# Performance work log

Hardware: AMD Instinct MI355X
Metric: run time of the kernel (lower is better)

The kernel has to match this reference:

```python
import jax, jax.numpy as jnp
import numpy as np

N = 4096
FEAT = 64


def _pairwise_dist(x):
    # x: [N, F] -> symmetric [N, N] Euclidean distance matrix, zero diagonal
    sq = jnp.sum(x * x, axis=-1)
    d2 = sq[:, None] + sq[None, :] - 2.0 * (x @ x.T)
    d = jnp.sqrt(jnp.maximum(d2, 0.0))
    return d * (1.0 - jnp.eye(x.shape[0], dtype=x.dtype))


def setup_inputs() -> dict:
    key = jax.random.key(0)
    k1, k2 = jax.random.split(key)
    x1 = jax.random.normal(k1, (N, FEAT), dtype=jnp.float32)
    x2 = jax.random.normal(k2, (N, FEAT), dtype=jnp.float32)
    return {"d1": _pairwise_dist(x1), "d2": _pairwise_dist(x2)}


def _mst_edges(d):
    # Prim's algorithm, O(N^2). For a distance matrix with generic (distinct)
    # entries the MST is unique and its N-1 edges are exactly the 0-dim
    # persistence pairs returned by the union-find PersistentHomologyCalculation.
    n = d.shape[0]
    INF = jnp.asarray(jnp.finfo(d.dtype).max, d.dtype)
    in_tree = jnp.zeros((n,), dtype=bool).at[0].set(True)
    min_dist = d[0]                       # best edge weight into the tree per node
    parent = jnp.zeros((n,), dtype=jnp.int32)  # tree endpoint of that best edge

    def step(carry, _):
        in_tree, min_dist, parent = carry
        masked = jnp.where(in_tree, INF, min_dist)
        j = jnp.argmin(masked).astype(jnp.int32)
        edge = jnp.stack([parent[j], j])  # (tree node, new node)
        in_tree = in_tree.at[j].set(True)
        dj = d[j]
        upd = (dj < min_dist) & (~in_tree)
        min_dist = jnp.where(upd, dj, min_dist)
        parent = jnp.where(upd, j, parent)
        return (in_tree, min_dist, parent), edge

    _, edges = jax.lax.scan(step, (in_tree, min_dist, parent), None, length=n - 1)
    return edges  # [N-1, 2] int32; d is symmetric so pair order is irrelevant


def reference(d1, d2):
    # Pairings are computed on detached CPU copies in the original -> no grad
    p1 = _mst_edges(jax.lax.stop_gradient(d1))
    p2 = jax.lax.stop_gradient(_mst_edges(jax.lax.stop_gradient(d2)))
    sig1 = d1[p1[:, 0], p1[:, 1]]
    sig2 = d2[p2[:, 0], p2[:, 1]]
    # match_edges == 'symmetric'
    sig1_2 = d2[p1[:, 0], p1[:, 1]]
    sig2_1 = d1[p2[:, 0], p2[:, 1]]
    return jnp.sum((sig1 - sig1_2) ** 2) + jnp.sum((sig2 - sig2_1) ** 2)
```

## Files before the change

kernel.cpp:

```cpp
#include <hip/hip_runtime.h>
#include <stdint.h>


#define N        4096
#define NROUNDS  12

typedef unsigned long long u64;
typedef uint32_t u32;

#define INFK (~0ull)

struct Ws {
    u64 best[2][N];
    u32 comp[2][N];
    u32 edges[2][N];
    u32 ncomp[2];
    u32 pad[14];
    u64 bm[2][N * 64];
};

__device__ __forceinline__ u64 umin64(u64 a, u64 b) { return a < b ? a : b; }

__device__ __forceinline__ u64 shfl_xor_u64(u64 x, int off) {
    u32 lo = (u32)x, hi = (u32)(x >> 32);
    lo = (u32)__shfl_xor((int)lo, off, 64);
    hi = (u32)__shfl_xor((int)hi, off, 64);
    return ((u64)hi << 32) | lo;
}

__launch_bounds__(256, 8)
__global__ void scanA_k(const float* __restrict__ d1, const float* __restrict__ d2,
                        Ws* __restrict__ ws) {
    const int m = blockIdx.x >> 10;
    const int wave = threadIdx.x >> 6, lane = threadIdx.x & 63;
    const int v = ((blockIdx.x & 1023) << 2) + wave;
    const float4* __restrict__ row4 = (const float4*)((m ? d2 : d1) + (size_t)v * N);

    const u32 uv = (u32)v;
    u64 bmin = INFK;
    #pragma unroll
    for (int j = 0; j < 16; ++j) {
        const int c = lane + 64 * j;
        float4 w = row4[c];
        const u32 c0 = (u32)(4 * c);
        if (c0 + 0 != uv) bmin = umin64(bmin, (((u64)__float_as_uint(w.x)) << 12) | (c0 + 0));
        if (c0 + 1 != uv) bmin = umin64(bmin, (((u64)__float_as_uint(w.y)) << 12) | (c0 + 1));
        if (c0 + 2 != uv) bmin = umin64(bmin, (((u64)__float_as_uint(w.z)) << 12) | (c0 + 2));
        if (c0 + 3 != uv) bmin = umin64(bmin, (((u64)__float_as_uint(w.w)) << 12) | (c0 + 3));
    }
    ws->bm[m][(size_t)v * 64 + lane] = bmin;

    u64 rowmin = bmin;
    #pragma unroll
    for (int off = 1; off <= 32; off <<= 1)
        rowmin = umin64(rowmin, shfl_xor_u64(rowmin, off));

    if (lane == 0) {
        u32 u  = (u32)rowmin & 0xFFFu;
        u64 wb = rowmin >> 12;
        u32 lo = min(uv, u), hi = max(uv, u);
        ws->best[m][v]  = (wb << 24) | ((u64)lo << 12) | (u64)hi;
        ws->comp[m][v]  = uv;
        ws->edges[m][v] = (uv << 12) | uv;
    }
    if (threadIdx.x == 0 && (blockIdx.x & 1023) == 0)
        ws->ncomp[m] = (u32)N;
}

__launch_bounds__(256, 8)
__global__ void scan2_k(const float* __restrict__ d1, const float* __restrict__ d2,
                        Ws* __restrict__ ws) {
    const int m = blockIdx.x >> 10;
    if (ws->ncomp[m] <= 1u) return;
    const int wave = threadIdx.x >> 6, lane = threadIdx.x & 63;
    const int v = ((blockIdx.x & 1023) << 2) + wave;

    const float* __restrict__ dm = m ? d2 : d1;
    const u32*   __restrict__ cm = ws->comp[m];
    u64* __restrict__ bmrow = ws->bm[m] + (size_t)v * 64;

    const u32 cv = cm[v];
    u64 key = bmrow[lane];
    bool cross = false;
    if (key != INFK) cross = (cm[(u32)key & 0xFFFu] != cv);

    u64 kb = cross ? key : INFK;
    #pragma unroll
    for (int off = 1; off <= 32; off <<= 1)
        kb = umin64(kb, shfl_xor_u64(kb, off));

    const bool need = (!cross) && (key < kb);
    u64 nm = INFK;
    if (need) {
        const float4* __restrict__ row4 = (const float4*)(dm + (size_t)v * N);
        const uint4*  __restrict__ c4   = (const uint4*)cm;
        #pragma unroll
        for (int j = 0; j < 16; ++j) {
            const int c = lane + 64 * j;
            float4 w = row4[c];
            uint4 cu = c4[c];
            u32 c0 = (u32)(4 * c);
            if (cu.x != cv) nm = umin64(nm, (((u64)__float_as_uint(w.x)) << 12) | (c0 + 0));
            if (cu.y != cv) nm = umin64(nm, (((u64)__float_as_uint(w.y)) << 12) | (c0 + 1));
            if (cu.z != cv) nm = umin64(nm, (((u64)__float_as_uint(w.z)) << 12) | (c0 + 2));
            if (cu.w != cv) nm = umin64(nm, (((u64)__float_as_uint(w.w)) << 12) | (c0 + 3));
        }
        bmrow[lane] = nm;
    }
    u64 kb2 = need ? nm : INFK;
    #pragma unroll
    for (int off = 1; off <= 32; off <<= 1)
        kb2 = umin64(kb2, shfl_xor_u64(kb2, off));

    u64 fin = umin64(kb, kb2);
    if (lane == 0 && fin != INFK) {
        u32 u  = (u32)fin & 0xFFFu;
        u64 wb = fin >> 12;
        u32 lo = min((u32)v, u), hi = max((u32)v, u);
        u64 g  = (wb << 24) | ((u64)lo << 12) | (u64)hi;
        if (g < ws->best[m][cv])
            atomicMin(&ws->best[m][cv], g);
    }
}

__launch_bounds__(256, 8)
__global__ void scanF_k(const float* __restrict__ d1, const float* __restrict__ d2,
                        Ws* __restrict__ ws, int first) {
    const int m = blockIdx.x >> 10;
    if (!first && ws->ncomp[m] <= 1u) return;
    const int wave = threadIdx.x >> 6, lane = threadIdx.x & 63;
    const int v = ((blockIdx.x & 1023) << 2) + wave;
    const float* __restrict__ dm = m ? d2 : d1;
    const u32*   __restrict__ cm = ws->comp[m];
    const float4* __restrict__ row4 = (const float4*)(dm + (size_t)v * N);
    const uint4*  __restrict__ c4   = (const uint4*)cm;
    const u32 cv = first ? (u32)v : cm[v];
    u64 kmin = INFK;
    #pragma unroll
    for (int j = 0; j < 16; ++j) {
        const int c = lane + 64 * j;
        float4 w = row4[c];
        uint4 cu;
        if (!first) cu = c4[c];
        const u32 c0 = (u32)(4 * c);
        bool x0, x1, x2, x3;
        if (first) {
            x0 = (c0+0 != cv); x1 = (c0+1 != cv); x2 = (c0+2 != cv); x3 = (c0+3 != cv);
        } else {
            x0 = (cu.x != cv); x1 = (cu.y != cv); x2 = (cu.z != cv); x3 = (cu.w != cv);
        }
        if (x0) kmin = umin64(kmin, (((u64)__float_as_uint(w.x)) << 12) | (c0 + 0));
        if (x1) kmin = umin64(kmin, (((u64)__float_as_uint(w.y)) << 12) | (c0 + 1));
        if (x2) kmin = umin64(kmin, (((u64)__float_as_uint(w.z)) << 12) | (c0 + 2));
        if (x3) kmin = umin64(kmin, (((u64)__float_as_uint(w.w)) << 12) | (c0 + 3));
    }
    #pragma unroll
    for (int off = 1; off <= 32; off <<= 1)
        kmin = umin64(kmin, shfl_xor_u64(kmin, off));
    if (lane == 0 && kmin != INFK) {
        u32 u  = (u32)kmin & 0xFFFu;
        u64 wb = kmin >> 12;
        u32 lo = min((u32)v, u), hi = max((u32)v, u);
        u64 g  = (wb << 24) | ((u64)lo << 12) | (u64)hi;
        if (first) {
            ws->best[m][v]  = g;
            ws->comp[m][v]  = (u32)v;
            ws->edges[m][v] = ((u32)v << 12) | (u32)v;
        } else if (g < ws->best[m][cv]) {
            atomicMin(&ws->best[m][cv], g);
        }
    }
    if (first && threadIdx.x == 0 && (blockIdx.x & 1023) == 0)
        ws->ncomp[m] = (u32)N;
}

__launch_bounds__(1024, 1)
__global__ void hook_k(const float* __restrict__ d1, const float* __restrict__ d2,
                       Ws* __restrict__ ws, float* __restrict__ out, int fin) {
    const int m = blockIdx.x;
    const int tid = threadIdx.x;
    const int lane = tid & 63, wave = tid >> 6;

    __shared__ u32 compL[N];
    __shared__ u32 nxtA[N];
    __shared__ u32 nxtB[N];
    __shared__ u32 red[16];
    __shared__ float fpart[16];

    if (ws->ncomp[m] > 1u) {
        u32* __restrict__ gcomp = ws->comp[m];
        u64* __restrict__ best  = ws->best[m];

        {
            uint4* dst = (uint4*)compL;
            const uint4* src = (const uint4*)gcomp;
            if (tid < N / 4) dst[tid] = src[tid];
        }
        __syncthreads();

        bool isroot[4];
        u64  bkey[4];

        #pragma unroll
        for (int k = 0; k < 4; ++k) {
            int i = tid + k * 1024;
            u32 x = (u32)i;
            bool r = (compL[i] == (u32)i);
            isroot[k] = r;
            u64 g = 0;
            if (r) {
                g = best[i];
                u32 lo = (u32)(g >> 12) & 0xFFFu;
                u32 hi = (u32)g & 0xFFFu;
                u32 cl = compL[lo], ch = compL[hi];
                x = (cl == (u32)i) ? ch : cl;
            }
            bkey[k] = g;
            nxtA[i] = x;
        }
        __syncthreads();

        #pragma unroll
        for (int k = 0; k < 4; ++k) {
            int i = tid + k * 1024;
            u32 nn = (u32)i;
            if (isroot[k]) {
                u32 o = nxtA[i];
                bool mutual = (nxtA[o] == (u32)i);
                nn = (mutual && ((u32)i < o)) ? (u32)i : o;
                if (nn != (u32)i)
                    ws->edges[m][i] = (u32)(bkey[k] & 0xFFFFFFu);
            }
            nxtB[i] = nn;
        }
        __syncthreads();

        for (int s = 0; s < 12; ++s) {
            u32 changed = 0;
            #pragma unroll
            for (int k = 0; k < 4; ++k) {
                int i = tid + k * 1024;
                u32 a = nxtB[i];
                u32 t = nxtB[a];
                if (t != a) changed = 1u;
                nxtB[i] = t;
            }
            if (!__syncthreads_or((int)changed)) break;
        }

        u32 cnt = 0;
        #pragma unroll
        for (int k = 0; k < 4; ++k) {
            int i = tid + k * 1024;
            if (isroot[k] && nxtB[i] == (u32)i) cnt++;
        }
        #pragma unroll
        for (int off = 32; off >= 1; off >>= 1) cnt += (u32)__shfl_down((int)cnt, off, 64);
        if (lane == 0) red[wave] = cnt;
        __syncthreads();

        #pragma unroll
        for (int k = 0; k < 4; ++k) {
            int i = tid + k * 1024;
            gcomp[i] = nxtB[compL[i]];
            if (isroot[k]) best[i] = INFK;
        }
        if (tid == 0) {
            u32 t = 0;
            #pragma unroll
            for (int w = 0; w < 16; ++w) t += red[w];
            ws->ncomp[m] = t;
        }
    }

    if (fin) {
        __syncthreads();
        float acc = 0.f;
        #pragma unroll
        for (int k = 0; k < 4; ++k) {
            int i = tid + k * 1024;
            u32 pk = ws->edges[m][i];
            u32 lo = (pk >> 12) & 0xFFFu, hi = pk & 0xFFFu;
            size_t off = (size_t)lo * N + hi;
            float df = d1[off] - d2[off];
            acc += df * df;
        }
        #pragma unroll
        for (int off = 32; off >= 1; off >>= 1) acc += __shfl_down(acc, off, 64);
        if (lane == 0) fpart[wave] = acc;
        __syncthreads();
        if (tid == 0) {
            float t = 0.f;
            #pragma unroll
            for (int w = 0; w < 16; ++w) t += fpart[w];
            atomicAdd(out, t);
        }
    }
}

extern "C" void kernel_launch(void* const* d_in, const int* in_sizes, int n_in,
                              void* d_out, int out_size, void* d_ws, size_t ws_size,
                              hipStream_t stream) {
    (void)in_sizes; (void)n_in; (void)out_size;
    const float* d1 = (const float*)d_in[0];
    const float* d2 = (const float*)d_in[1];
    float* out = (float*)d_out;
    Ws* ws = (Ws*)d_ws;
    const bool big = (ws_size >= sizeof(Ws));

    hipMemsetAsync(d_out, 0, sizeof(float), stream);
    for (int r = 0; r < NROUNDS; ++r) {
        if (big) {
            if (r == 0) scanA_k<<<dim3(2048), dim3(256), 0, stream>>>(d1, d2, ws);
            else        scan2_k<<<dim3(2048), dim3(256), 0, stream>>>(d1, d2, ws);
        } else {
            scanF_k<<<dim3(2048), dim3(256), 0, stream>>>(d1, d2, ws, r == 0 ? 1 : 0);
        }
        hook_k<<<dim3(2), dim3(1024), 0, stream>>>(d1, d2, ws, out, r == NROUNDS - 1 ? 1 : 0);
    }
}
```

Before: 262.7 us.

## Track compact root list so hook kernel only processes live components

The Boruvka hook kernel now keeps a global list of component roots and their count, and iterates only over those roots instead of all N vertices each round. First-round initialisation of comp and edges moves from the scan kernels into the hook kernel via a new first flag. The large shared-memory arrays are collapsed into a single nxt array. This cuts per-round work in the single-block hook as components merge. In exchange the root list is built with shared atomics, and the fixed myroot[4] buffer assumes at most 4 roots per thread.

After: 267.7 us. Within noise of the previous version (+1.9%).

```diff
diff --git a/kernel.cpp b/kernel.cpp
--- a/kernel.cpp
+++ b/kernel.cpp
@@ -15,7 +15,9 @@
     u32 comp[2][N];
     u32 edges[2][N];
     u32 ncomp[2];
-    u32 pad[14];
+    u32 rootcnt[2];
+    u32 pad[12];
+    u32 rootlist[2][N];
     u64 bm[2][N * 64];
 };
 
@@ -59,12 +61,8 @@
         u32 u  = (u32)rowmin & 0xFFFu;
         u64 wb = rowmin >> 12;
         u32 lo = min(uv, u), hi = max(uv, u);
-        ws->best[m][v]  = (wb << 24) | ((u64)lo << 12) | (u64)hi;
-        ws->comp[m][v]  = uv;
-        ws->edges[m][v] = (uv << 12) | uv;
-    }
-    if (threadIdx.x == 0 && (blockIdx.x & 1023) == 0)
-        ws->ncomp[m] = (u32)N;
+        ws->best[m][v] = (wb << 24) | ((u64)lo << 12) | (u64)hi;
+    }
 }
 
 __launch_bounds__(256, 8)
@@ -162,115 +160,91 @@
         u64 wb = kmin >> 12;
         u32 lo = min((u32)v, u), hi = max((u32)v, u);
         u64 g  = (wb << 24) | ((u64)lo << 12) | (u64)hi;
-        if (first) {
-            ws->best[m][v]  = g;
-            ws->comp[m][v]  = (u32)v;
-            ws->edges[m][v] = ((u32)v << 12) | (u32)v;
-        } else if (g < ws->best[m][cv]) {
-            atomicMin(&ws->best[m][cv], g);
-        }
-    }
-    if (first && threadIdx.x == 0 && (blockIdx.x & 1023) == 0)
-        ws->ncomp[m] = (u32)N;
+        if (first) ws->best[m][v] = g;
+        else if (g < ws->best[m][cv]) atomicMin(&ws->best[m][cv], g);
+    }
 }
 
 __launch_bounds__(1024, 1)
 __global__ void hook_k(const float* __restrict__ d1, const float* __restrict__ d2,
-                       Ws* __restrict__ ws, float* __restrict__ out, int fin) {
+                       Ws* __restrict__ ws, float* __restrict__ out,
+                       int first, int fin) {
     const int m = blockIdx.x;
     const int tid = threadIdx.x;
     const int lane = tid & 63, wave = tid >> 6;
 
-    __shared__ u32 compL[N];
-    __shared__ u32 nxtA[N];
-    __shared__ u32 nxtB[N];
-    __shared__ u32 red[16];
+    __shared__ u32 nxt[N];
+    __shared__ u32 cnt_sh;
     __shared__ float fpart[16];
 
-    if (ws->ncomp[m] > 1u) {
-        u32* __restrict__ gcomp = ws->comp[m];
-        u64* __restrict__ best  = ws->best[m];
-
-        {
-            uint4* dst = (uint4*)compL;
-            const uint4* src = (const uint4*)gcomp;
-            if (tid < N / 4) dst[tid] = src[tid];
-        }
-        __syncthreads();
-
-        bool isroot[4];
-        u64  bkey[4];
-
-        #pragma unroll
-        for (int k = 0; k < 4; ++k) {
-            int i = tid + k * 1024;
-            u32 x = (u32)i;
-            bool r = (compL[i] == (u32)i);
-            isroot[k] = r;
-            u64 g = 0;
-            if (r) {
-                g = best[i];
-                u32 lo = (u32)(g >> 12) & 0xFFFu;
-                u32 hi = (u32)g & 0xFFFu;
-                u32 cl = compL[lo], ch = compL[hi];
-                x = (cl == (u32)i) ? ch : cl;
-            }
-            bkey[k] = g;
-            nxtA[i] = x;
-        }
-        __syncthreads();
-
-        #pragma unroll
-        for (int k = 0; k < 4; ++k) {
-            int i = tid + k * 1024;
-            u32 nn = (u32)i;
-            if (isroot[k]) {
-                u32 o = nxtA[i];
-                bool mutual = (nxtA[o] == (u32)i);
-                nn = (mutual && ((u32)i < o)) ? (u32)i : o;
-                if (nn != (u32)i)
-                    ws->edges[m][i] = (u32)(bkey[k] & 0xFFFFFFu);
-            }
-            nxtB[i] = nn;
+    u32* __restrict__ cm   = ws->comp[m];
+    u64* __restrict__ best = ws->best[m];
+    u32* __restrict__ rl   = ws->rootlist[m];
+
+    const bool alive = first || (ws->ncomp[m] > 1u);
+    if (alive) {
+        const u32 nr = first ? (u32)N : ws->rootcnt[m];
+
+        for (u32 t = tid; t < nr; t += 1024) {
+            u32 i = first ? t : rl[t];
+            u64 g = best[i];
+            u32 x = i;
+            if (g != INFK) {
+                u32 lo = (u32)(g >> 12) & 0xFFFu, hi = (u32)g & 0xFFFu;
+                u32 cl = first ? lo : cm[lo];
+                u32 ch = first ? hi : cm[hi];
+                x = (cl == i) ? ch : cl;
+            }
+            nxt[i] = x;
+        }
+        __syncthreads();
+
+        for (u32 t = tid; t < nr; t += 1024) {
+            u32 i = first ? t : rl[t];
+            u32 o = nxt[i];
+            bool die = false;
+            if (o != i) {
+                bool mutual = (nxt[o] == i);
+                if (mutual && i < o) nxt[i] = i;
+                else die = true;
+            }
+            if (die)             ws->edges[m][i] = (u32)(best[i] & 0xFFFFFFu);
+            else if (first)      ws->edges[m][i] = (i << 12) | i;
         }
         __syncthreads();
 
         for (int s = 0; s < 12; ++s) {
             u32 changed = 0;
-            #pragma unroll
-            for (int k = 0; k < 4; ++k) {
-                int i = tid + k * 1024;
-                u32 a = nxtB[i];
-                u32 t = nxtB[a];
-                if (t != a) changed = 1u;
-                nxtB[i] = t;
+            for (u32 t = tid; t < nr; t += 1024) {
+                u32 i = first ? t : rl[t];
+                u32 a = nxt[i];
+                u32 b2 = nxt[a];
+                if (b2 != a) changed = 1u;
+                nxt[i] = b2;
             }
             if (!__syncthreads_or((int)changed)) break;
         }
 
-        u32 cnt = 0;
-        #pragma unroll
-        for (int k = 0; k < 4; ++k) {
-            int i = tid + k * 1024;
-            if (isroot[k] && nxtB[i] == (u32)i) cnt++;
-        }
-        #pragma unroll
-        for (int off = 32; off >= 1; off >>= 1) cnt += (u32)__shfl_down((int)cnt, off, 64);
-        if (lane == 0) red[wave] = cnt;
-        __syncthreads();
-
-        #pragma unroll
-        for (int k = 0; k < 4; ++k) {
-            int i = tid + k * 1024;
-            gcomp[i] = nxtB[compL[i]];
-            if (isroot[k]) best[i] = INFK;
-        }
-        if (tid == 0) {
-            u32 t = 0;
-            #pragma unroll
-            for (int w = 0; w < 16; ++w) t += red[w];
-            ws->ncomp[m] = t;
-        }
+        u32 myroot[4];
+        int nm_ = 0;
+        for (u32 t = tid; t < nr; t += 1024) myroot[nm_++] = first ? t : rl[t];
+        if (tid == 0) cnt_sh = 0;
+        __syncthreads();
+
+        for (int q = 0; q < nm_; ++q) {
+            u32 i = myroot[q];
+            if (nxt[i] == i) {
+                u32 p = atomicAdd(&cnt_sh, 1u);
+                rl[p] = i;
+                best[i] = INFK;
+            }
+        }
+        for (u32 t = tid; t < (u32)N; t += 1024) {
+            u32 co = first ? t : cm[t];
+            cm[t] = nxt[co];
+        }
+        __syncthreads();
+        if (tid == 0) { ws->ncomp[m] = cnt_sh; ws->rootcnt[m] = cnt_sh; }
     }
 
     if (fin) {
@@ -316,6 +290,8 @@
         } else {
             scanF_k<<<dim3(2048), dim3(256), 0, stream>>>(d1, d2, ws, r == 0 ? 1 : 0);
         }
-        hook_k<<<dim3(2), dim3(1024), 0, stream>>>(d1, d2, ws, out, r == NROUNDS - 1 ? 1 : 0);
-    }
-}
+        hook_k<<<dim3(2), dim3(1024), 0, stream>>>(d1, d2, ws, out,
+                                                   r == 0 ? 1 : 0,
+                                                   r == NROUNDS - 1 ? 1 : 0);
+    }
+}
```
